# Kernel optimization log

Measured on AMD Instinct MI355X. Metric: run time of the kernel, lower is better.

## Reference

```python
import jax, jax.numpy as jnp
import numpy as np

V, E, H, K, S, B = 32000, 256, 256, 3, 2048, 4


def setup_inputs() -> dict:
    key = jax.random.key(0)
    k0, k1, k2, k3 = jax.random.split(key, 4)
    tokens_seq = jax.random.randint(k0, (S, B), 0, V)              # (seq_len, batch)
    embed = jax.random.normal(k1, (V, E), dtype=jnp.float32) * 0.02
    w1 = jax.random.normal(k2, (K * E, H), dtype=jnp.float32) / np.sqrt(K * E).astype(np.float32)
    b1 = jnp.zeros((H,), dtype=jnp.float32)
    w2 = jax.random.normal(k3, (H, V), dtype=jnp.float32) / np.sqrt(H).astype(np.float32)
    b2 = jnp.zeros((V,), dtype=jnp.float32)
    return {"tokens_seq": tokens_seq, "embed": embed, "w1": w1, "b1": b1, "w2": w2, "b2": b2}


def reference(tokens_seq, embed, w1, b1, w2, b2):
    # tokens_seq: (S, B) int. Context at position t = last K tokens, left-padded with token id 0.
    seq_len, batch = tokens_seq.shape
    padded = jnp.concatenate([jnp.zeros((K, batch), tokens_seq.dtype), tokens_seq], axis=0)  # (S+K, B)
    win_idx = jnp.arange(seq_len)[:, None] + jnp.arange(K)[None, :]   # (S, K): rows t..t+K-1 of padded == tokens[t-K:t]
    ctx = padded[win_idx]                      # (S, K, B)
    ctx = jnp.transpose(ctx, (0, 2, 1))        # (S, B, K)
    # one-hot @ embed.weight == gather
    emb = embed[ctx]                           # (S, B, K, E)
    x = emb.reshape(seq_len, batch, K * E)     # flatten k-gram window
    h = jax.nn.silu(x @ w1 + b1)               # (S, B, H)
    logits = h @ w2 + b2                       # (S, B, V)
    return logits
```

## Files before the change

kernel.cpp:

```cpp
#include <hip/hip_runtime.h>
#include <hip/hip_bf16.h>
#include <stdint.h>

#define V 32000
#define E 256
#define H 256
#define KCTX 3
#define S 2048
#define B 4
#define M (S * B)
#define K1 (KCTX * E)

typedef __attribute__((ext_vector_type(8))) short s16x8;
typedef __attribute__((ext_vector_type(4))) short s16x4;
typedef __attribute__((ext_vector_type(4))) float f32x4;

typedef const __attribute__((address_space(1))) unsigned short* gas_t;
typedef __attribute__((address_space(3))) unsigned short* las_t;

static __device__ __forceinline__ unsigned short f2bf(float f) {
  union { float f; unsigned u; } v; v.f = f;
  unsigned u = v.u;
  unsigned r = (u + 0x7fffu + ((u >> 16) & 1u)) >> 16;
  return (unsigned short)r;
}

__global__ void k_transpose_cast(const float* __restrict__ in,
                                 unsigned short* __restrict__ out,
                                 int R, int C) {
  __shared__ float tile[32][33];
  int bx = blockIdx.x;
  int by = blockIdx.y;
  int tx = threadIdx.x & 31;
  int ty = threadIdx.x >> 5;
#pragma unroll
  for (int i = 0; i < 32; i += 8)
    tile[ty + i][tx] = in[(size_t)(by * 32 + ty + i) * C + bx * 32 + tx];
  __syncthreads();
#pragma unroll
  for (int i = 0; i < 32; i += 8)
    out[(size_t)(bx * 32 + ty + i) * R + by * 32 + tx] = f2bf(tile[tx][ty + i]);
}

__global__ __launch_bounds__(256) void k_stage1(
    const int* __restrict__ tok, const float* __restrict__ embed,
    const unsigned short* __restrict__ w1T,
    const float* __restrict__ b1, unsigned short* __restrict__ hbuf) {
  __shared__ unsigned short xlds[16][K1 + 8];
  __shared__ int toks[48];
  int bid = blockIdx.x;
  int t = threadIdx.x;
  int m0 = bid * 16;

  if (t < 48) {
    int r = t / 3, kk = t - r * 3;
    int m = m0 + r, s = m >> 2, bb = m & 3;
    int tp = s - KCTX + kk;
    toks[t] = (tp >= 0) ? tok[tp * B + bb] : 0;
  }
  __syncthreads();

#pragma unroll
  for (int j = 0; j < 12; j++) {
    int c = j * 256 + t;
    int r = c / 192;
    int cc = c - r * 192;
    int kk = cc >> 6;
    int e4 = cc & 63;
    f32x4 v = *reinterpret_cast<const f32x4*>(
        embed + (size_t)toks[r * 3 + kk] * E + e4 * 4);
    s16x4 o;
#pragma unroll
    for (int jj = 0; jj < 4; jj++) o[jj] = (short)f2bf(v[jj]);
    *reinterpret_cast<s16x4*>(&xlds[r][cc * 4]) = o;
  }
  __syncthreads();

  int l = t & 63;
  int wv = t >> 6;
  int n0 = wv * 64;

  f32x4 zero = {0.f, 0.f, 0.f, 0.f};
  f32x4 acc[4];
#pragma unroll
  for (int ni = 0; ni < 4; ni++) acc[ni] = zero;

#pragma unroll
  for (int kt = 0; kt < 24; kt++) {
    s16x8 a = *reinterpret_cast<const s16x8*>(&xlds[l & 15][kt * 32 + (l >> 4) * 8]);
#pragma unroll
    for (int ni = 0; ni < 4; ni++) {
      int n = n0 + ni * 16 + (l & 15);
      s16x8 bf = *reinterpret_cast<const s16x8*>(
          w1T + (size_t)n * K1 + kt * 32 + (l >> 4) * 8);
      acc[ni] = __builtin_amdgcn_mfma_f32_16x16x32_bf16(a, bf, acc[ni], 0, 0, 0);
    }
  }

  int rbase = m0 + (l >> 4) * 4;
#pragma unroll
  for (int ni = 0; ni < 4; ni++) {
    int n = n0 + ni * 16 + (l & 15);
    float bias = b1[n];
#pragma unroll
    for (int j = 0; j < 4; j++) {
      float vv = acc[ni][j] + bias;
      float sv = vv / (1.0f + __expf(-vv));
      hbuf[(size_t)(rbase + j) * H + n] = f2bf(sv);
    }
  }
}

__global__ __launch_bounds__(512, 4) void k_stage2(
    const unsigned short* __restrict__ hbuf,
    const unsigned short* __restrict__ w2T,
    const float* __restrict__ b2, float* __restrict__ out) {
  __shared__ unsigned short lds[2][12288];

  int bid = blockIdx.x;
  int xcd = bid & 7;
  int i = bid >> 3;
  int mtile = xcd * 4 + (i & 3);
  int ntile = i >> 2;
  int m_base = mtile * 256, n_base = ntile * 128;

  int t = threadIdx.x;
  int l = t & 63;
  int wv = t >> 6;
  int wm = wv >> 1, wn = wv & 1;

  int srow = l >> 2;
  int c4 = l & 3;

  f32x4 zero = {0.f, 0.f, 0.f, 0.f};
  f32x4 acc[4][4];
#pragma unroll
  for (int mi = 0; mi < 4; mi++)
#pragma unroll
    for (int ni = 0; ni < 4; ni++) acc[mi][ni] = zero;

  auto stage = [&](int tt, int p) {
    int gk = tt * 32;
#pragma unroll
    for (int j = 0; j < 2; j++) {
      int r0 = wv * 32 + j * 16;
      int row = r0 + srow;
      int gc = c4 ^ ((row >> 1) & 3);
      const unsigned short* ga =
          hbuf + (size_t)(m_base + row) * 256 + gk + gc * 8;
      __builtin_amdgcn_global_load_lds((gas_t)ga, (las_t)&lds[p][r0 * 32], 16, 0, 0);
    }
    {
      int r0 = wv * 16;
      int row = r0 + srow;
      int gc = c4 ^ ((row >> 1) & 3);
      const unsigned short* gb =
          w2T + (size_t)(n_base + row) * 256 + gk + gc * 8;
      __builtin_amdgcn_global_load_lds((gas_t)gb, (las_t)&lds[p][8192 + r0 * 32], 16, 0, 0);
    }
  };

  auto compute = [&](int p) {
    const unsigned short* bufA = &lds[p][0];
    const unsigned short* bufB = &lds[p][8192];
    int c = l >> 4;
    s16x8 af[4], bfr[4];
#pragma unroll
    for (int mi = 0; mi < 4; mi++) {
      int row = wm * 64 + mi * 16 + (l & 15);
      af[mi] = *reinterpret_cast<const s16x8*>(
          bufA + row * 32 + (c ^ ((row >> 1) & 3)) * 8);
    }
#pragma unroll
    for (int ni = 0; ni < 4; ni++) {
      int row = wn * 64 + ni * 16 + (l & 15);
      bfr[ni] = *reinterpret_cast<const s16x8*>(
          bufB + row * 32 + (c ^ ((row >> 1) & 3)) * 8);
    }
#pragma unroll
    for (int mi = 0; mi < 4; mi++)
#pragma unroll
      for (int ni = 0; ni < 4; ni++)
        acc[mi][ni] = __builtin_amdgcn_mfma_f32_16x16x32_bf16(
            af[mi], bfr[ni], acc[mi][ni], 0, 0, 0);
  };

  stage(0, 0);
  __syncthreads();
#pragma unroll
  for (int tt = 0; tt < 8; tt++) {
    if (tt < 7) stage(tt + 1, (tt + 1) & 1);
    compute(tt & 1);
    __syncthreads();
  }
  __syncthreads();

  float* fpatch = reinterpret_cast<float*>(&lds[0][0]) + wv * 1088;
  int q = l >> 4, r = l & 15;
  float bias[4];
#pragma unroll
  for (int ni = 0; ni < 4; ni++)
    bias[ni] = b2[n_base + wn * 64 + ni * 16 + r];

#pragma unroll
  for (int mi = 0; mi < 4; mi++) {
#pragma unroll
    for (int ni = 0; ni < 4; ni++)
#pragma unroll
      for (int j = 0; j < 4; j++)
        fpatch[(q * 4 + j) * 68 + ni * 16 + r] = acc[mi][ni][j] + bias[ni];
#pragma unroll
    for (int it = 0; it < 4; it++) {
      int row16 = it * 4 + q;
      f32x4 v = *reinterpret_cast<const f32x4*>(fpatch + row16 * 68 + r * 4);
      float* dst = &out[(size_t)(m_base + wm * 64 + mi * 16 + row16) * V +
                        n_base + wn * 64 + r * 4];
      __builtin_nontemporal_store(v, reinterpret_cast<f32x4*>(dst));
    }
  }
}

extern "C" void kernel_launch(void* const* d_in, const int* in_sizes, int n_in,
                              void* d_out, int out_size, void* d_ws,
                              size_t ws_size, hipStream_t stream) {
  const int* tokens = (const int*)d_in[0];
  const float* embed = (const float*)d_in[1];
  const float* w1 = (const float*)d_in[2];
  const float* b1 = (const float*)d_in[3];
  const float* w2 = (const float*)d_in[4];
  const float* b2 = (const float*)d_in[5];
  float* out = (float*)d_out;

  unsigned short* w2T = (unsigned short*)d_ws;
  unsigned short* w1T = w2T + (size_t)V * E;
  unsigned short* hb  = w1T + (size_t)H * K1;

  k_transpose_cast<<<dim3(V / 32, H / 32), 256, 0, stream>>>(w2, w2T, H, V);
  k_transpose_cast<<<dim3(H / 32, K1 / 32), 256, 0, stream>>>(w1, w1T, K1, H);
  k_stage1<<<512, 256, 0, stream>>>(tokens, embed, w1T, b1, hb);
  k_stage2<<<8000, 512, 0, stream>>>(hb, w2T, b2, out);
}
```

Before: 270.9 us.

## Merge w2 transpose into stage1 launch and streamline stage2 fragment loads

Folds the w2 transpose-cast into the stage-1 kernel as extra blocks, so one launch handles both and the separate transpose launch goes away. In stage2 the global and LDS addresses are precomputed once outside the loop with the swizzle hoisted, and the fragment loads are interleaved with the MFMAs in two halves so fewer B fragments are live at once. The occupancy hint is raised from 4 to 6 waves per EU, which may force register spilling.

```diff
diff --git a/kernel.cpp b/kernel.cpp
--- a/kernel.cpp
+++ b/kernel.cpp
@@ -42,15 +42,33 @@
     out[(size_t)(bx * 32 + ty + i) * R + by * 32 + tx] = f2bf(tile[tx][ty + i]);
 }
 
-__global__ __launch_bounds__(256) void k_stage1(
+__global__ __launch_bounds__(256) void k_prep(
     const int* __restrict__ tok, const float* __restrict__ embed,
-    const unsigned short* __restrict__ w1T,
-    const float* __restrict__ b1, unsigned short* __restrict__ hbuf) {
-  __shared__ unsigned short xlds[16][K1 + 8];
-  __shared__ int toks[48];
+    const unsigned short* __restrict__ w1T, const float* __restrict__ b1,
+    unsigned short* __restrict__ hbuf,
+    const float* __restrict__ w2, unsigned short* __restrict__ w2T) {
+  __shared__ __align__(16) char smem[25088];
   int bid = blockIdx.x;
   int t = threadIdx.x;
-  int m0 = bid * 16;
+
+  if (bid < 8000) {
+    float(*tile)[33] = reinterpret_cast<float(*)[33]>(smem);
+    int bx = bid % 1000, by = bid / 1000;
+    int tx = t & 31, ty = t >> 5;
+#pragma unroll
+    for (int i = 0; i < 32; i += 8)
+      tile[ty + i][tx] = w2[(size_t)(by * 32 + ty + i) * V + bx * 32 + tx];
+    __syncthreads();
+#pragma unroll
+    for (int i = 0; i < 32; i += 8)
+      w2T[(size_t)(bx * 32 + ty + i) * H + by * 32 + tx] = f2bf(tile[tx][ty + i]);
+    return;
+  }
+
+  unsigned short(*xlds)[K1 + 8] =
+      reinterpret_cast<unsigned short(*)[K1 + 8]>(smem);
+  int* toks = reinterpret_cast<int*>(smem + 16 * (K1 + 8) * 2);
+  int m0 = (bid - 8000) * 16;
 
   if (t < 48) {
     int r = t / 3, kk = t - r * 3;
@@ -111,7 +129,7 @@
   }
 }
 
-__global__ __launch_bounds__(512, 4) void k_stage2(
+__global__ __launch_bounds__(512, 6) void k_stage2(
     const unsigned short* __restrict__ hbuf,
     const unsigned short* __restrict__ w2T,
     const float* __restrict__ b2, float* __restrict__ out) {
@@ -131,6 +149,17 @@
 
   int srow = l >> 2;
   int c4 = l & 3;
+  int sswz = (srow >> 1) & 3;
+
+  const unsigned short* ha =
+      hbuf + (size_t)(m_base + wv * 32 + srow) * 256 + (c4 ^ sswz) * 8;
+  const unsigned short* hb =
+      w2T + (size_t)(n_base + wv * 16 + srow) * 256 + (c4 ^ sswz) * 8;
+
+  int cswz = ((l & 15) >> 1) & 3;
+  int ck = l >> 4;
+  int a_off = (wm * 64 + (l & 15)) * 32 + ((ck ^ cswz) * 8);
+  int b_off = 8192 + (wn * 64 + (l & 15)) * 32 + ((ck ^ cswz) * 8);
 
   f32x4 zero = {0.f, 0.f, 0.f, 0.f};
   f32x4 acc[4][4];
@@ -140,49 +169,31 @@
     for (int ni = 0; ni < 4; ni++) acc[mi][ni] = zero;
 
   auto stage = [&](int tt, int p) {
-    int gk = tt * 32;
-#pragma unroll
-    for (int j = 0; j < 2; j++) {
-      int r0 = wv * 32 + j * 16;
-      int row = r0 + srow;
-      int gc = c4 ^ ((row >> 1) & 3);
-      const unsigned short* ga =
-          hbuf + (size_t)(m_base + row) * 256 + gk + gc * 8;
-      __builtin_amdgcn_global_load_lds((gas_t)ga, (las_t)&lds[p][r0 * 32], 16, 0, 0);
-    }
-    {
-      int r0 = wv * 16;
-      int row = r0 + srow;
-      int gc = c4 ^ ((row >> 1) & 3);
-      const unsigned short* gb =
-          w2T + (size_t)(n_base + row) * 256 + gk + gc * 8;
-      __builtin_amdgcn_global_load_lds((gas_t)gb, (las_t)&lds[p][8192 + r0 * 32], 16, 0, 0);
-    }
+#pragma unroll
+    for (int j = 0; j < 2; j++)
+      __builtin_amdgcn_global_load_lds((gas_t)(ha + tt * 32 + j * 4096),
+                                       (las_t)&lds[p][(wv * 32 + j * 16) * 32],
+                                       16, 0, 0);
+    __builtin_amdgcn_global_load_lds((gas_t)(hb + tt * 32),
+                                     (las_t)&lds[p][8192 + (wv * 16) * 32],
+                                     16, 0, 0);
   };
 
   auto compute = [&](int p) {
-    const unsigned short* bufA = &lds[p][0];
-    const unsigned short* bufB = &lds[p][8192];
-    int c = l >> 4;
-    s16x8 af[4], bfr[4];
-#pragma unroll
-    for (int mi = 0; mi < 4; mi++) {
-      int row = wm * 64 + mi * 16 + (l & 15);
-      af[mi] = *reinterpret_cast<const s16x8*>(
-          bufA + row * 32 + (c ^ ((row >> 1) & 3)) * 8);
-    }
-#pragma unroll
-    for (int ni = 0; ni < 4; ni++) {
-      int row = wn * 64 + ni * 16 + (l & 15);
-      bfr[ni] = *reinterpret_cast<const s16x8*>(
-          bufB + row * 32 + (c ^ ((row >> 1) & 3)) * 8);
-    }
-#pragma unroll
-    for (int mi = 0; mi < 4; mi++)
-#pragma unroll
-      for (int ni = 0; ni < 4; ni++)
-        acc[mi][ni] = __builtin_amdgcn_mfma_f32_16x16x32_bf16(
-            af[mi], bfr[ni], acc[mi][ni], 0, 0, 0);
+    const unsigned short* base = &lds[p][0];
+#pragma unroll
+    for (int half = 0; half < 2; half++) {
+      s16x8 bf0 = *reinterpret_cast<const s16x8*>(base + b_off + (half * 2) * 512);
+      s16x8 bf1 = *reinterpret_cast<const s16x8*>(base + b_off + (half * 2 + 1) * 512);
+#pragma unroll
+      for (int mi = 0; mi < 4; mi++) {
+        s16x8 af = *reinterpret_cast<const s16x8*>(base + a_off + mi * 512);
+        acc[mi][half * 2] =
+            __builtin_amdgcn_mfma_f32_16x16x32_bf16(af, bf0, acc[mi][half * 2], 0, 0, 0);
+        acc[mi][half * 2 + 1] =
+            __builtin_amdgcn_mfma_f32_16x16x32_bf16(af, bf1, acc[mi][half * 2 + 1], 0, 0, 0);
+      }
+    }
   };
 
   stage(0, 0);
@@ -235,8 +246,7 @@
   unsigned short* w1T = w2T + (size_t)V * E;
   unsigned short* hb  = w1T + (size_t)H * K1;
 
-  k_transpose_cast<<<dim3(V / 32, H / 32), 256, 0, stream>>>(w2, w2T, H, V);
   k_transpose_cast<<<dim3(H / 32, K1 / 32), 256, 0, stream>>>(w1, w1T, K1, H);
-  k_stage1<<<512, 256, 0, stream>>>(tokens, embed, w1T, b1, hb);
+  k_prep<<<8512, 256, 0, stream>>>(tokens, embed, w1T, b1, hb, w2, w2T);
   k_stage2<<<8000, 512, 0, stream>>>(hb, w2T, b2, out);
 }
```

After: 992.8 us. 3.66x slower.
